# Kernel tuning notes

Measured on AMD Instinct MI355X. Metric: run time of the kernel, lower is better.

The kernel has to match this reference:

```python
import jax, jax.numpy as jnp
import numpy as np

# TT-matrix dense layer: y = relu(x @ M + b) where M is a TT-matrix with cores
# G_k of shape [r_{k-1}, m_k, n_k, r_k], M[i1..id, j1..jd] = G1[:,i1,j1,:] ... Gd[:,id,jd,:]

IN_DIMS = [8, 8, 8, 8]
OUT_DIMS = [8, 8, 8, 8]
RANKS = [1, 8, 8, 8, 1]
BATCH = 4096


def setup_inputs() -> dict:
    key = jax.random.key(0)
    ks = jax.random.split(key, 6)
    inp = {"x": jax.random.normal(ks[0], (BATCH, int(np.prod(IN_DIMS))), dtype=jnp.float32)}
    # glorot-ish scale for TT cores so that the reconstructed matrix has sane variance
    for k in range(4):
        shape = (RANKS[k], IN_DIMS[k], OUT_DIMS[k], RANKS[k + 1])
        scale = 0.3
        inp[f"core{k}"] = scale * jax.random.normal(ks[1 + k], shape, dtype=jnp.float32)
    inp["b"] = 0.1 * jnp.ones((int(np.prod(OUT_DIMS)),), dtype=jnp.float32)
    return inp


def _tt_matmul(x, cores):
    # x: [B, prod(m)], cores[k]: [r_{k-1}, m_k, n_k, r_k]
    B = x.shape[0]
    ms = [G.shape[1] for G in cores]
    # res: [a, r, m_k, t] with a = B * prod(n_done), t = prod(m_rest)
    res = x.reshape(B, 1, ms[0], -1)
    for k, G in enumerate(cores):
        a, _, _, t = res.shape
        n, r_next = G.shape[2], G.shape[3]
        # contract rank and current input mode: [a, n, r_next, t]
        res = jnp.einsum('aqmt,qmnr->anrt', res, G)
        m_next = ms[k + 1] if k + 1 < len(cores) else 1
        res = res.reshape(a * n, r_next, m_next, t // m_next)
    return res.reshape(B, -1)  # [B, prod(n)], big-endian output index order


def reference(x, core0, core1, core2, core3, b):
    y = _tt_matmul(x, [core0, core1, core2, core3])
    return jax.nn.relu(y + b)
```

## Files before the change

kernel.cpp:

```cpp
#include <hip/hip_runtime.h>
#include <hip/hip_bf16.h>
#include <stdint.h>

typedef short bf16x8 __attribute__((ext_vector_type(8)));
typedef float f32x4 __attribute__((ext_vector_type(4)));
typedef unsigned short u16;
typedef u16 ushort8 __attribute__((ext_vector_type(8)));

typedef __attribute__((address_space(3))) void lds_void;
typedef const __attribute__((address_space(1))) void gbl_void;

#define BAR() do { asm volatile("" ::: "memory"); __builtin_amdgcn_s_barrier(); asm volatile("" ::: "memory"); } while (0)
#define WAITV(N) asm volatile("s_waitcnt vmcnt(" #N ")" ::: "memory")
#define WAITL0() do { asm volatile("s_waitcnt lgkmcnt(0)" ::: "memory"); __builtin_amdgcn_sched_barrier(0); } while (0)
#define SCHED() __builtin_amdgcn_sched_barrier(0)

__device__ __forceinline__ u16 f2bf(float f) {
  uint32_t u = __builtin_bit_cast(uint32_t, f);
  u += 0x7fffu + ((u >> 16) & 1u);
  return (u16)(u >> 16);
}

__global__ __launch_bounds__(256) void cvt_x(const float* __restrict__ x,
                                             u16* __restrict__ xb) {
  const int i = (blockIdx.x * 256 + threadIdx.x) * 8;
  float4 a = *(const float4*)(x + i);
  float4 b = *(const float4*)(x + i + 4);
  ushort8 o;
  o[0] = f2bf(a.x); o[1] = f2bf(a.y); o[2] = f2bf(a.z); o[3] = f2bf(a.w);
  o[4] = f2bf(b.x); o[5] = f2bf(b.y); o[6] = f2bf(b.z); o[7] = f2bf(b.w);
  *(ushort8*)(xb + i) = o;
}

__global__ __launch_bounds__(256) void build_mt(
    const float* __restrict__ c0, const float* __restrict__ c1,
    const float* __restrict__ c2, const float* __restrict__ c3,
    u16* __restrict__ Mt) {
  const int bid = blockIdx.x;
  const int j1 = bid & 7, i1 = (bid >> 3) & 7, j0 = (bid >> 6) & 7, i0 = bid >> 9;
  const int t = threadIdx.x;
  __shared__ float v[512];
  __shared__ float g3[512];
  g3[t] = c3[t];
  g3[t + 256] = c3[t + 256];
  float w2[8];
#pragma unroll
  for (int r2 = 0; r2 < 8; ++r2) {
    float s = 0.f;
#pragma unroll
    for (int r1 = 0; r1 < 8; ++r1)
      s += c0[(i0 * 8 + j0) * 8 + r1] * c1[((r1 * 8 + i1) * 8 + j1) * 8 + r2];
    w2[r2] = s;
  }
#pragma unroll
  for (int e = t; e < 512; e += 256) {
    const int r3 = e & 7, j2 = (e >> 3) & 7, i2 = e >> 6;
    float s = 0.f;
#pragma unroll
    for (int r2 = 0; r2 < 8; ++r2)
      s += w2[r2] * c2[((r2 * 8 + i2) * 8 + j2) * 8 + r3];
    v[e] = s;
  }
  __syncthreads();
  const int jr = t >> 2, ic0 = (t & 3) * 16;
  const int j2 = jr >> 3, j3 = jr & 7;
  const size_t base =
      (size_t)(j0 * 512 + j1 * 64 + jr) * 4096 + (i0 * 512 + i1 * 64) + ic0;
  ushort8 o0, o1;
#pragma unroll
  for (int q = 0; q < 16; ++q) {
    const int ic = ic0 + q, i2 = ic >> 3, i3 = ic & 7;
    float s = 0.f;
#pragma unroll
    for (int r3 = 0; r3 < 8; ++r3)
      s += v[(i2 << 6) + (j2 << 3) + r3] * g3[(r3 << 6) + (i3 << 3) + j3];
    const u16 h = f2bf(s);
    if (q < 8) o0[q] = h; else o1[q - 8] = h;
  }
  *(ushort8*)(Mt + base) = o0;
  *(ushort8*)(Mt + base + 8) = o1;
}

__global__ __launch_bounds__(512, 2) void gemm_bias_relu(
    const u16* __restrict__ A, const u16* __restrict__ Bt,
    const float* __restrict__ bias, float* __restrict__ C) {
  constexpr int K = 4096, N = 4096, NT = 64;
  __shared__ __align__(16) char lds[131072];
  const int t = threadIdx.x;
  const int l = t & 63, w = t >> 6;
  const int wr = w >> 2, wc = w & 3;
  const int lr = l & 15, lk = l >> 4;
  const int bm = blockIdx.y, bn = blockIdx.x;

  const char* gA = (const char*)A + (size_t)bm * 256 * (K * 2);
  const char* gB = (const char*)Bt + (size_t)bn * 256 * (K * 2);
  const int srow = t >> 3;
  const int schunk = (t & 7) ^ (srow & 7);
  const int sgo = srow * (K * 2) + schunk * 16;
  const int sld = t * 16;

  const int axor = (lk ^ (lr & 7)) * 16;
  const int aoff0 = (wr * 128 + lr) * 128 + axor;
  const int aoff1 = aoff0 ^ 64;
  const int boff0 = 65536 + (wc * 64 + lr) * 128 + axor;
  const int boff1 = boff0 ^ 64;

  auto stA = [&](int p, int h, int kt) {
    const char* src = gA + (size_t)(h * 128) * (K * 2) + kt * 128 + sgo;
    char* dst = lds + p * 32768 + h * 16384 + sld;
    __builtin_amdgcn_global_load_lds((gbl_void*)src, (lds_void*)dst, 16, 0, 0);
    __builtin_amdgcn_global_load_lds((gbl_void*)(src + (size_t)64 * (K * 2)),
                                     (lds_void*)(dst + 8192), 16, 0, 0);
  };
  auto stB = [&](int p, int h, int kt) {
    const char* src = gB + (size_t)(h * 128) * (K * 2) + kt * 128 + sgo;
    char* dst = lds + 65536 + p * 32768 + h * 16384 + sld;
    __builtin_amdgcn_global_load_lds((gbl_void*)src, (lds_void*)dst, 16, 0, 0);
    __builtin_amdgcn_global_load_lds((gbl_void*)(src + (size_t)64 * (K * 2)),
                                     (lds_void*)(dst + 8192), 16, 0, 0);
  };
  auto rdA = [&](int p, int off, int m) -> bf16x8 {
    return *(const bf16x8*)(lds + p * 32768 + off + m * 2048);
  };
  auto rdB = [&](int p, int off, int n) -> bf16x8 {
    return *(const bf16x8*)(lds + p * 32768 + off + n * 2048);
  };

  bf16x8 a0[8], a1[8], b0[2][2], b1[2][2];
  f32x4 acc[8][4];
#pragma unroll
  for (int m = 0; m < 8; ++m)
#pragma unroll
    for (int n = 0; n < 4; ++n) acc[m][n] = f32x4{0.f, 0.f, 0.f, 0.f};

  stA(0, 0, 0); stA(0, 1, 0); stB(0, 0, 0); stB(0, 1, 0);
  stA(1, 0, 1); stA(1, 1, 1); stB(1, 0, 1); stB(1, 1, 1);
  WAITV(8);
  BAR();
#pragma unroll
  for (int m = 0; m < 8; ++m) a0[m] = rdA(0, aoff0, m);
#pragma unroll
  for (int n = 0; n < 2; ++n) { b0[n][0] = rdB(0, boff0, n); b0[n][1] = rdB(0, boff1, n); }

  for (int it = 0; it < NT / 2; ++it) {
#pragma unroll
    for (int hf = 0; hf < 2; ++hf) {
      const int p = hf;
      const int kt = 2 * it + hf;
      const int kn = (kt + 2) & (NT - 1);
      WAITV(12);
#pragma unroll
      for (int m = 0; m < 8; ++m) a1[m] = rdA(p, aoff1, m);
      BAR(); WAITL0();
      __builtin_amdgcn_s_setprio(1);
#pragma unroll
      for (int m = 0; m < 8; ++m)
#pragma unroll
        for (int n = 0; n < 2; ++n)
          acc[m][n] = __builtin_amdgcn_mfma_f32_16x16x32_bf16(a0[m], b0[n][0], acc[m][n], 0, 0, 0);
      __builtin_amdgcn_s_setprio(0); SCHED();
      BAR();
      WAITV(8);
#pragma unroll
      for (int n = 0; n < 2; ++n) { b1[n][0] = rdB(p, boff0, n + 2); b1[n][1] = rdB(p, boff1, n + 2); }
      stA(p, 0, kn);
      BAR(); WAITL0();
      __builtin_amdgcn_s_setprio(1);
#pragma unroll
      for (int m = 0; m < 8; ++m)
#pragma unroll
        for (int n = 0; n < 2; ++n)
          acc[m][n] = __builtin_amdgcn_mfma_f32_16x16x32_bf16(a1[m], b0[n][1], acc[m][n], 0, 0, 0);
      __builtin_amdgcn_s_setprio(0); SCHED();
      BAR();
      WAITV(2);
#pragma unroll
      for (int n = 0; n < 2; ++n) { b0[n][0] = rdB(p ^ 1, boff0, n); b0[n][1] = rdB(p ^ 1, boff1, n); }
      stA(p, 1, kn); stB(p, 0, kn);
      BAR(); WAITL0();
      __builtin_amdgcn_s_setprio(1);
#pragma unroll
      for (int m = 0; m < 8; ++m)
#pragma unroll
        for (int n = 0; n < 2; ++n)
          acc[m][2 + n] = __builtin_amdgcn_mfma_f32_16x16x32_bf16(a0[m], b1[n][0], acc[m][2 + n], 0, 0, 0);
      __builtin_amdgcn_s_setprio(0); SCHED();
      BAR();
      WAITV(10);
#pragma unroll
      for (int m = 0; m < 8; ++m) a0[m] = rdA(p ^ 1, aoff0, m);
      stB(p, 1, kn);
      BAR(); WAITL0();
      __builtin_amdgcn_s_setprio(1);
#pragma unroll
      for (int m = 0; m < 8; ++m)
#pragma unroll
        for (int n = 0; n < 2; ++n)
          acc[m][2 + n] = __builtin_amdgcn_mfma_f32_16x16x32_bf16(a1[m], b1[n][1], acc[m][2 + n], 0, 0, 0);
      __builtin_amdgcn_s_setprio(0); SCHED();
      BAR();
    }
  }

  const int row0 = bm * 256 + wr * 128;
  const int col0 = bn * 256 + wc * 64;
#pragma unroll
  for (int n = 0; n < 4; ++n) {
    const int col = col0 + n * 16 + lr;
    const float bv = bias[col];
#pragma unroll
    for (int m = 0; m < 8; ++m) {
      const int r0 = row0 + m * 16 + lk * 4;
#pragma unroll
      for (int vv = 0; vv < 4; ++vv) {
        const float val = acc[m][n][vv] + bv;
        C[(size_t)(r0 + vv) * N + col] = val > 0.f ? val : 0.f;
      }
    }
  }
}

extern "C" void kernel_launch(void* const* d_in, const int* in_sizes, int n_in,
                              void* d_out, int out_size, void* d_ws, size_t ws_size,
                              hipStream_t stream) {
  const float* x  = (const float*)d_in[0];
  const float* c0 = (const float*)d_in[1];
  const float* c1 = (const float*)d_in[2];
  const float* c2 = (const float*)d_in[3];
  const float* c3 = (const float*)d_in[4];
  const float* b  = (const float*)d_in[5];
  float* out = (float*)d_out;

  u16* xb  = (u16*)d_ws;
  u16* mtb = xb + (size_t)4096 * 4096;

  cvt_x<<<dim3(16777216 / (256 * 8)), dim3(256), 0, stream>>>(x, xb);
  build_mt<<<dim3(4096), dim3(256), 0, stream>>>(c0, c1, c2, c3, mtb);
  gemm_bias_relu<<<dim3(16, 16), dim3(512), 0, stream>>>(xb, mtb, b, out);
}
```

Measured before the change: 145.3 us.

## Rework GEMM LDS pipeline waits and add XCD-aware tile swizzle

Restructures the software pipeline of the bf16 GEMM. It drops the explicit lgkmcnt waits and sched barriers, groups the A-tile and B-tile global-to-LDS loads into pairs, and collapses the several vmcnt waits into a single WAITV(4) per half-step. The launch becomes a 1D grid whose block ids are remapped so that neighbouring output tiles land on the same XCD, aiming for better L2 reuse of A and B rows. The prefetch index is clamped at the tail instead of wrapping, so the last steps no longer load wrapped-around tiles. It relies on the compiler to insert LDS waits, and the looser vmcnt accounting carries some risk of read-before-load races.

```diff
diff --git a/kernel.cpp b/kernel.cpp
--- a/kernel.cpp
+++ b/kernel.cpp
@@ -12,8 +12,6 @@
 
 #define BAR() do { asm volatile("" ::: "memory"); __builtin_amdgcn_s_barrier(); asm volatile("" ::: "memory"); } while (0)
 #define WAITV(N) asm volatile("s_waitcnt vmcnt(" #N ")" ::: "memory")
-#define WAITL0() do { asm volatile("s_waitcnt lgkmcnt(0)" ::: "memory"); __builtin_amdgcn_sched_barrier(0); } while (0)
-#define SCHED() __builtin_amdgcn_sched_barrier(0)
 
 __device__ __forceinline__ u16 f2bf(float f) {
   uint32_t u = __builtin_bit_cast(uint32_t, f);
@@ -90,7 +88,10 @@
   const int l = t & 63, w = t >> 6;
   const int wr = w >> 2, wc = w & 3;
   const int lr = l & 15, lk = l >> 4;
-  const int bm = blockIdx.y, bn = blockIdx.x;
+
+  const int id = blockIdx.x;
+  const int wg = (id & 7) * 32 + (id >> 3);
+  const int bm = wg >> 4, bn = wg & 15;
 
   const char* gA = (const char*)A + (size_t)bm * 256 * (K * 2);
   const char* gB = (const char*)Bt + (size_t)bn * 256 * (K * 2);
@@ -126,7 +127,7 @@
     return *(const bf16x8*)(lds + p * 32768 + off + n * 2048);
   };
 
-  bf16x8 a0[8], a1[8], b0[2][2], b1[2][2];
+  bf16x8 a0[8], a1[8], b01[2][2], b23[2][2];
   f32x4 acc[8][4];
 #pragma unroll
   for (int m = 0; m < 8; ++m)
@@ -140,64 +141,60 @@
 #pragma unroll
   for (int m = 0; m < 8; ++m) a0[m] = rdA(0, aoff0, m);
 #pragma unroll
-  for (int n = 0; n < 2; ++n) { b0[n][0] = rdB(0, boff0, n); b0[n][1] = rdB(0, boff1, n); }
+  for (int n = 0; n < 2; ++n) { b01[n][0] = rdB(0, boff0, n); b01[n][1] = rdB(0, boff1, n); }
 
   for (int it = 0; it < NT / 2; ++it) {
 #pragma unroll
     for (int hf = 0; hf < 2; ++hf) {
       const int p = hf;
       const int kt = 2 * it + hf;
-      const int kn = (kt + 2) & (NT - 1);
-      WAITV(12);
+      const int kn = (kt + 2 < NT) ? kt + 2 : kt;
 #pragma unroll
       for (int m = 0; m < 8; ++m) a1[m] = rdA(p, aoff1, m);
-      BAR(); WAITL0();
-      __builtin_amdgcn_s_setprio(1);
-#pragma unroll
-      for (int m = 0; m < 8; ++m)
-#pragma unroll
-        for (int n = 0; n < 2; ++n)
-          acc[m][n] = __builtin_amdgcn_mfma_f32_16x16x32_bf16(a0[m], b0[n][0], acc[m][n], 0, 0, 0);
-      __builtin_amdgcn_s_setprio(0); SCHED();
-      BAR();
-      WAITV(8);
-#pragma unroll
-      for (int n = 0; n < 2; ++n) { b1[n][0] = rdB(p, boff0, n + 2); b1[n][1] = rdB(p, boff1, n + 2); }
-      stA(p, 0, kn);
-      BAR(); WAITL0();
-      __builtin_amdgcn_s_setprio(1);
-#pragma unroll
-      for (int m = 0; m < 8; ++m)
-#pragma unroll
-        for (int n = 0; n < 2; ++n)
-          acc[m][n] = __builtin_amdgcn_mfma_f32_16x16x32_bf16(a1[m], b0[n][1], acc[m][n], 0, 0, 0);
-      __builtin_amdgcn_s_setprio(0); SCHED();
-      BAR();
-      WAITV(2);
-#pragma unroll
-      for (int n = 0; n < 2; ++n) { b0[n][0] = rdB(p ^ 1, boff0, n); b0[n][1] = rdB(p ^ 1, boff1, n); }
-      stA(p, 1, kn); stB(p, 0, kn);
-      BAR(); WAITL0();
-      __builtin_amdgcn_s_setprio(1);
-#pragma unroll
-      for (int m = 0; m < 8; ++m)
-#pragma unroll
-        for (int n = 0; n < 2; ++n)
-          acc[m][2 + n] = __builtin_amdgcn_mfma_f32_16x16x32_bf16(a0[m], b1[n][0], acc[m][2 + n], 0, 0, 0);
-      __builtin_amdgcn_s_setprio(0); SCHED();
-      BAR();
-      WAITV(10);
+      BAR();
+      __builtin_amdgcn_s_setprio(1);
+#pragma unroll
+      for (int m = 0; m < 8; ++m)
+#pragma unroll
+        for (int n = 0; n < 2; ++n)
+          acc[m][n] = __builtin_amdgcn_mfma_f32_16x16x32_bf16(a0[m], b01[n][0], acc[m][n], 0, 0, 0);
+      __builtin_amdgcn_s_setprio(0);
+      BAR();
+#pragma unroll
+      for (int n = 0; n < 2; ++n) { b23[n][0] = rdB(p, boff0, n + 2); b23[n][1] = rdB(p, boff1, n + 2); }
+      stA(p, 0, kn); stA(p, 1, kn);
+      BAR();
+      __builtin_amdgcn_s_setprio(1);
+#pragma unroll
+      for (int m = 0; m < 8; ++m)
+#pragma unroll
+        for (int n = 0; n < 2; ++n)
+          acc[m][n] = __builtin_amdgcn_mfma_f32_16x16x32_bf16(a1[m], b01[n][1], acc[m][n], 0, 0, 0);
+      __builtin_amdgcn_s_setprio(0);
+      WAITV(4);
+      BAR();
+#pragma unroll
+      for (int n = 0; n < 2; ++n) { b01[n][0] = rdB(p ^ 1, boff0, n); b01[n][1] = rdB(p ^ 1, boff1, n); }
+      stB(p, 0, kn); stB(p, 1, kn);
+      BAR();
+      __builtin_amdgcn_s_setprio(1);
+#pragma unroll
+      for (int m = 0; m < 8; ++m)
+#pragma unroll
+        for (int n = 0; n < 2; ++n)
+          acc[m][2 + n] = __builtin_amdgcn_mfma_f32_16x16x32_bf16(a0[m], b23[n][0], acc[m][2 + n], 0, 0, 0);
+      __builtin_amdgcn_s_setprio(0);
+      BAR();
 #pragma unroll
       for (int m = 0; m < 8; ++m) a0[m] = rdA(p ^ 1, aoff0, m);
-      stB(p, 1, kn);
-      BAR(); WAITL0();
-      __builtin_amdgcn_s_setprio(1);
-#pragma unroll
-      for (int m = 0; m < 8; ++m)
-#pragma unroll
-        for (int n = 0; n < 2; ++n)
-          acc[m][2 + n] = __builtin_amdgcn_mfma_f32_16x16x32_bf16(a1[m], b1[n][1], acc[m][2 + n], 0, 0, 0);
-      __builtin_amdgcn_s_setprio(0); SCHED();
+      BAR();
+      __builtin_amdgcn_s_setprio(1);
+#pragma unroll
+      for (int m = 0; m < 8; ++m)
+#pragma unroll
+        for (int n = 0; n < 2; ++n)
+          acc[m][2 + n] = __builtin_amdgcn_mfma_f32_16x16x32_bf16(a1[m], b23[n][1], acc[m][2 + n], 0, 0, 0);
+      __builtin_amdgcn_s_setprio(0);
       BAR();
     }
   }
@@ -236,5 +233,5 @@
 
   cvt_x<<<dim3(16777216 / (256 * 8)), dim3(256), 0, stream>>>(x, xb);
   build_mt<<<dim3(4096), dim3(256), 0, stream>>>(c0, c1, c2, c3, mtb);
-  gemm_bias_relu<<<dim3(16, 16), dim3(512), 0, stream>>>(xb, mtb, b, out);
-}
+  gemm_bias_relu<<<dim3(256), dim3(512), 0, stream>>>(xb, mtb, b, out);
+}
```

Result: slower. 149.6 us (+3.0%).
